# Kernel optimization log

Hardware: AMD Instinct MI355X
Metric: run time of the kernel (lower is better)

Reference implementation:

```python
import jax, jax.numpy as jnp
import numpy as np

RANK = 16
LN_EPS = 1e-5


def _layer_norm(x, eps=LN_EPS):
    mu = jnp.mean(x, axis=-1, keepdims=True)
    var = jnp.var(x, axis=-1, keepdims=True)
    return (x - mu) / jnp.sqrt(var + eps)


def setup_inputs() -> dict:
    key = jax.random.key(0)
    ks = jax.random.split(key, 8)
    B, S, D, M, R = 32, 4096, 160, 16, RANK
    query = jax.random.normal(ks[0], (B, S, D), dtype=jnp.float32)
    interface = jax.random.normal(ks[1], (B, S, D), dtype=jnp.float32)
    memory = jax.random.normal(ks[2], (B, M, D), dtype=jnp.float32)
    sd = 1.0 / np.sqrt(D)
    sr = 1.0 / np.sqrt(R)
    # torch nn.Linear weights: [out_features, in_features]
    W_read_key = jax.random.uniform(ks[3], (R, D), minval=-sd, maxval=sd, dtype=jnp.float32)
    W_read_value = jax.random.uniform(ks[4], (D, R), minval=-sr, maxval=sr, dtype=jnp.float32)
    W_write_key = jax.random.uniform(ks[5], (R, D), minval=-sd, maxval=sd, dtype=jnp.float32)
    W_write_erase = jax.random.uniform(ks[6], (D, R), minval=-sr, maxval=sr, dtype=jnp.float32)
    W_write_add = jax.random.uniform(ks[7], (D, R), minval=-sr, maxval=sr, dtype=jnp.float32)
    return {
        "query": query,
        "interface": interface,
        "memory": memory,
        "W_read_key": W_read_key,
        "W_read_value": W_read_value,
        "W_write_key": W_write_key,
        "W_write_erase": W_write_erase,
        "W_write_add": W_write_add,
    }


def reference(query, interface, memory, W_read_key, W_read_value,
              W_write_key, W_write_erase, W_write_add):
    R = RANK
    # ---- read ----
    q_proj = jnp.einsum('bsd,rd->bsr', query, W_read_key)          # [B,S,R]
    mem_proj = memory[..., :R]                                      # [B,M,R]
    scores = jnp.einsum('bsr,bmr->bsm', q_proj, mem_proj) / jnp.sqrt(jnp.float32(R))
    attn = jax.nn.softmax(scores, axis=-1)                          # [B,S,M]
    content = jnp.einsum('bsm,bmd->bsd', attn, memory)              # [B,S,D]
    read_out = jnp.einsum('bsr,dr->bsd', content[..., :R], W_read_value)
    # ---- write ----
    i_mean = jnp.mean(interface, axis=1)                            # [B,D]
    i_proj = jnp.einsum('bd,rd->br', i_mean, W_write_key)           # [B,R]
    erase = jax.nn.sigmoid(jnp.einsum('br,dr->bd', i_proj, W_write_erase))[:, None, :]
    add = jnp.einsum('br,dr->bd', i_proj, W_write_add)[:, None, :]
    new_memory = _layer_norm(memory * (1.0 - erase) + add)          # [B,M,D]
    return read_out, new_memory
```

## Files before the change

kernel.cpp:

```cpp
#include <hip/hip_runtime.h>
#include <hip/hip_bf16.h>
#include <math.h>

#define NB 32
#define NS 4096
#define ND 160
#define ND4 40
#define NM 16
#define NR 16
#define TPB 128
#define NCB (NS / TPB)

typedef float  f32x4  __attribute__((ext_vector_type(4)));
typedef short  bf16x8 __attribute__((ext_vector_type(8)));
typedef unsigned int u32x4 __attribute__((ext_vector_type(4)));

__device__ __forceinline__ unsigned bfpair(float lo, float hi) {
    union { float f; unsigned u; } a, c;
    a.f = lo; c.f = hi;
    unsigned ua = (a.u + 0x7FFFu + ((a.u >> 16) & 1u)) >> 16;
    unsigned uc = (c.u + 0x7FFFu + ((c.u >> 16) & 1u)) >> 16;
    return (uc << 16) | (ua & 0xFFFFu);
}

__device__ __forceinline__ bf16x8 mkfrag(unsigned w0, unsigned w1,
                                         unsigned w2, unsigned w3) {
    union { u32x4 u; bf16x8 h; } x;
    x.u = (u32x4){w0, w1, w2, w3};
    return x.h;
}

__global__ __launch_bounds__(256) void ulm_read_kernel(
    const float* __restrict__ query,
    const float* __restrict__ iface,
    const float* __restrict__ memory,
    const float* __restrict__ Wrk,
    const float* __restrict__ Wrv,
    float* __restrict__ read_out,
    float* __restrict__ ipart)
{
    __shared__ __align__(16) float sKV[2 * NM * ND];
    __shared__ float sM16[NM * NR];
    __shared__ unsigned sP[4][16 * 10];
    __shared__ float4 sIred[4 * ND4];

    const int t = threadIdx.x;
    const int chunk = blockIdx.x;
    const int b = blockIdx.y;
    const int s0 = chunk * TPB;
    const int w  = t >> 6;
    const int l  = t & 63;
    const int lr = l & 15;
    const int lg = l >> 4;

    sM16[t] = memory[((size_t)b * NM + (t >> 4)) * ND + (t & 15)];
    __syncthreads();

    if (t < ND) {
        float wk[NR], wv[NR];
#pragma unroll
        for (int r = 0; r < NR; ++r) wk[r] = Wrk[r * ND + t];
        const float4* wrv4 = reinterpret_cast<const float4*>(Wrv + t * NR);
#pragma unroll
        for (int j = 0; j < 4; ++j) {
            float4 v = wrv4[j];
            wv[j * 4 + 0] = v.x; wv[j * 4 + 1] = v.y;
            wv[j * 4 + 2] = v.z; wv[j * 4 + 3] = v.w;
        }
#pragma unroll
        for (int m = 0; m < NM; ++m) {
            float aK = 0.f, aV = 0.f;
#pragma unroll
            for (int r = 0; r < NR; ++r) {
                float mv = sM16[m * NR + r];
                aK += mv * wk[r];
                aV += mv * wv[r];
            }
            sKV[m * ND + t]           = aK * 0.25f;
            sKV[NM * ND + m * ND + t] = aV;
        }
    }
    __syncthreads();

    bf16x8 kf[5];
#pragma unroll
    for (int kb = 0; kb < 5; ++kb) {
        const float* src = &sKV[lr * ND + lg * 8 + kb * 32];
        float4 a = *reinterpret_cast<const float4*>(src);
        float4 c = *reinterpret_cast<const float4*>(src + 4);
        kf[kb] = mkfrag(bfpair(a.x, a.y), bfpair(a.z, a.w),
                        bfpair(c.x, c.y), bfpair(c.z, c.w));
    }

    bf16x8 vf[10];
#pragma unroll
    for (int d = 0; d < 10; ++d) {
        if (lg < 2) {
            float f0 = sKV[NM*ND + (lg*8 + 0) * ND + d*16 + lr];
            float f1 = sKV[NM*ND + (lg*8 + 1) * ND + d*16 + lr];
            float f2 = sKV[NM*ND + (lg*8 + 2) * ND + d*16 + lr];
            float f3 = sKV[NM*ND + (lg*8 + 3) * ND + d*16 + lr];
            float f4 = sKV[NM*ND + (lg*8 + 4) * ND + d*16 + lr];
            float f5 = sKV[NM*ND + (lg*8 + 5) * ND + d*16 + lr];
            float f6 = sKV[NM*ND + (lg*8 + 6) * ND + d*16 + lr];
            float f7 = sKV[NM*ND + (lg*8 + 7) * ND + d*16 + lr];
            vf[d] = mkfrag(bfpair(f0, f1), bfpair(f2, f3),
                           bfpair(f4, f5), bfpair(f6, f7));
        } else {
            vf[d] = mkfrag(0u, 0u, 0u, 0u);
        }
    }

    const size_t base = (size_t)b * NS * ND;
    const float4* q4  = reinterpret_cast<const float4*>(query + base) + (size_t)s0 * ND4;
    float4* out4      = reinterpret_cast<float4*>(read_out + base) + (size_t)s0 * ND4;
    const int wtok0 = w * 32;
    unsigned* pl = &sP[w][0];

#pragma unroll 1
    for (int set = 0; set < 2; ++set) {
        const int tok = wtok0 + set * 16 + lr;

        float4 qr[10];
#pragma unroll
        for (int kb = 0; kb < 5; ++kb) {
            qr[2*kb]   = q4[(size_t)tok * ND4 + lg * 2 + kb * 8];
            qr[2*kb+1] = q4[(size_t)tok * ND4 + lg * 2 + kb * 8 + 1];
        }

        f32x4 D = {0.f, 0.f, 0.f, 0.f};
#pragma unroll
        for (int kb = 0; kb < 5; ++kb) {
            bf16x8 qf = mkfrag(bfpair(qr[2*kb].x,   qr[2*kb].y),
                               bfpair(qr[2*kb].z,   qr[2*kb].w),
                               bfpair(qr[2*kb+1].x, qr[2*kb+1].y),
                               bfpair(qr[2*kb+1].z, qr[2*kb+1].w));
            D = __builtin_amdgcn_mfma_f32_16x16x32_bf16(kf[kb], qf, D, 0, 0, 0);
        }

        float mx = fmaxf(fmaxf(D[0], D[1]), fmaxf(D[2], D[3]));
        mx = fmaxf(mx, __shfl_xor(mx, 16));
        mx = fmaxf(mx, __shfl_xor(mx, 32));
        float e0 = __expf(D[0] - mx), e1 = __expf(D[1] - mx);
        float e2 = __expf(D[2] - mx), e3 = __expf(D[3] - mx);
        float sm = e0 + e1 + e2 + e3;
        sm += __shfl_xor(sm, 16);
        sm += __shfl_xor(sm, 32);
        float inv = 1.f / sm;
        e0 *= inv; e1 *= inv; e2 *= inv; e3 *= inv;

        pl[lr * 10 + lg * 2 + 0] = bfpair(e0, e1);
        pl[lr * 10 + lg * 2 + 1] = bfpair(e2, e3);
        asm volatile("s_waitcnt lgkmcnt(0)" ::: "memory");
        int pb = (lg < 2) ? (lr * 10 + lg * 4) : 0;
        bf16x8 pf = mkfrag(pl[pb], pl[pb + 1], pl[pb + 2], pl[pb + 3]);

#pragma unroll
        for (int d = 0; d < 10; ++d) {
            f32x4 D2 = {0.f, 0.f, 0.f, 0.f};
            D2 = __builtin_amdgcn_mfma_f32_16x16x32_bf16(vf[d], pf, D2, 0, 0, 0);
            out4[(size_t)tok * ND4 + d * 4 + lg] =
                make_float4(D2[0], D2[1], D2[2], D2[3]);
        }
    }

    const float4* i4 = reinterpret_cast<const float4*>(iface + base) + (size_t)s0 * ND4;
    const int l8 = l & 7, g8 = l >> 3;
    float4 ia[5];
#pragma unroll
    for (int k = 0; k < 5; ++k) ia[k] = make_float4(0.f, 0.f, 0.f, 0.f);
#pragma unroll
    for (int i = 0; i < 4; ++i) {
        int tk = wtok0 + g8 * 4 + i;
#pragma unroll
        for (int k = 0; k < 5; ++k) {
            float4 v = i4[(size_t)tk * ND4 + l8 + 8 * k];
            ia[k].x += v.x; ia[k].y += v.y; ia[k].z += v.z; ia[k].w += v.w;
        }
    }
#pragma unroll
    for (int k = 0; k < 5; ++k) {
        float x = ia[k].x, y = ia[k].y, z = ia[k].z, u = ia[k].w;
#pragma unroll
        for (int off = 8; off <= 32; off <<= 1) {
            x += __shfl_xor(x, off); y += __shfl_xor(y, off);
            z += __shfl_xor(z, off); u += __shfl_xor(u, off);
        }
        if (l < 8) sIred[w * ND4 + k * 8 + l8] = make_float4(x, y, z, u);
    }
    __syncthreads();
    if (t < ND4) {
        float4 a0 = sIred[t], a1 = sIred[ND4 + t];
        float4 a2 = sIred[2 * ND4 + t], a3 = sIred[3 * ND4 + t];
        float4 tot = make_float4(a0.x + a1.x + a2.x + a3.x,
                                 a0.y + a1.y + a2.y + a3.y,
                                 a0.z + a1.z + a2.z + a3.z,
                                 a0.w + a1.w + a2.w + a3.w);
        reinterpret_cast<float4*>(ipart + ((size_t)(b * NCB + chunk)) * ND)[t] = tot;
    }
}

__global__ __launch_bounds__(256) void ulm_write_kernel(
    const float* __restrict__ memory,
    const float* __restrict__ Wwk,
    const float* __restrict__ Wwe,
    const float* __restrict__ Wwa,
    const float* __restrict__ ipart,
    float* __restrict__ new_mem)
{
    __shared__ float sIm[ND];
    __shared__ float sIp[NR];
    __shared__ float sOmE[ND];
    __shared__ float sAdd[ND];

    const int b = blockIdx.x;
    const int t = threadIdx.x;

    if (t < ND) {
        float acc = 0.f;
#pragma unroll 8
        for (int c = 0; c < NCB; ++c)
            acc += ipart[((size_t)(b * NCB + c)) * ND + t];
        sIm[t] = acc * (1.0f / NS);
    }
    __syncthreads();

    if (t < NR) {
        float acc = 0.f;
        for (int d = 0; d < ND; ++d) acc += sIm[d] * Wwk[t * ND + d];
        sIp[t] = acc;
    }
    __syncthreads();

    if (t < ND) {
        float e = 0.f, a = 0.f;
#pragma unroll
        for (int r = 0; r < NR; ++r) {
            float ip = sIp[r];
            e += ip * Wwe[t * NR + r];
            a += ip * Wwa[t * NR + r];
        }
        sOmE[t] = 1.0f - 1.0f / (1.0f + __expf(-e));
        sAdd[t] = a;
    }
    __syncthreads();

    const int wave = t >> 6, lane = t & 63;
    for (int m = wave; m < NM; m += 4) {
        const float* mrow = memory + ((size_t)b * NM + m) * ND;
        float v0 = mrow[lane] * sOmE[lane] + sAdd[lane];
        float v1 = mrow[lane + 64] * sOmE[lane + 64] + sAdd[lane + 64];
        float v2 = 0.f;
        const bool has2 = lane < 32;
        if (has2) v2 = mrow[lane + 128] * sOmE[lane + 128] + sAdd[lane + 128];
        float s  = v0 + v1 + v2;
        float sq = v0 * v0 + v1 * v1 + v2 * v2;
#pragma unroll
        for (int off = 32; off; off >>= 1) {
            s  += __shfl_xor(s, off);
            sq += __shfl_xor(sq, off);
        }
        float mu   = s * (1.0f / ND);
        float var  = sq * (1.0f / ND) - mu * mu;
        float rstd = rsqrtf(var + 1e-5f);
        float* orow = new_mem + ((size_t)b * NM + m) * ND;
        orow[lane]      = (v0 - mu) * rstd;
        orow[lane + 64] = (v1 - mu) * rstd;
        if (has2) orow[lane + 128] = (v2 - mu) * rstd;
    }
}

extern "C" void kernel_launch(void* const* d_in, const int* in_sizes, int n_in,
                              void* d_out, int out_size, void* d_ws, size_t ws_size,
                              hipStream_t stream) {
    const float* query  = (const float*)d_in[0];
    const float* iface  = (const float*)d_in[1];
    const float* memory = (const float*)d_in[2];
    const float* Wrk    = (const float*)d_in[3];
    const float* Wrv    = (const float*)d_in[4];
    const float* Wwk    = (const float*)d_in[5];
    const float* Wwe    = (const float*)d_in[6];
    const float* Wwa    = (const float*)d_in[7];

    float* read_out = (float*)d_out;
    float* new_mem  = (float*)d_out + (size_t)NB * NS * ND;
    float* ipart    = (float*)d_ws;

    dim3 grid1(NCB, NB);
    ulm_read_kernel<<<grid1, 256, 0, stream>>>(query, iface, memory, Wrk, Wrv,
                                               read_out, ipart);
    ulm_write_kernel<<<NB, 256, 0, stream>>>(memory, Wwk, Wwe, Wwa, ipart, new_mem);
}
```

Before: 56.66 us.

## Hoist K/V fragment folding into a prologue kernel and halve tokens per block

Per-batch folding of memory with the read weights into bf16 MFMA fragments moves into a separate small kernel that writes them to workspace. The main read kernel now loads the prebuilt fragments directly instead of recomputing and converting them in every block. Each block handles 64 tokens with one 16-token set per wave, and the interface loads are issued before the output MFMAs. This removes redundant per-block prologue work and syncs and doubles the block count, at the cost of an extra launch, more workspace and more partial sums for the write kernel to reduce.

```diff
diff --git a/kernel.cpp b/kernel.cpp
--- a/kernel.cpp
+++ b/kernel.cpp
@@ -8,7 +8,7 @@
 #define ND4 40
 #define NM 16
 #define NR 16
-#define TPB 128
+#define TPB 64
 #define NCB (NS / TPB)
 
 typedef float  f32x4  __attribute__((ext_vector_type(4)));
@@ -23,6 +23,10 @@
     return (uc << 16) | (ua & 0xFFFFu);
 }
 
+__device__ __forceinline__ bf16x8 asfrag(u32x4 u) {
+    union { u32x4 u; bf16x8 h; } x; x.u = u; return x.h;
+}
+
 __device__ __forceinline__ bf16x8 mkfrag(unsigned w0, unsigned w1,
                                          unsigned w2, unsigned w3) {
     union { u32x4 u; bf16x8 h; } x;
@@ -30,17 +34,70 @@
     return x.h;
 }
 
+__global__ __launch_bounds__(256) void ulm_fold_kv(
+    const float* __restrict__ memory,
+    const float* __restrict__ Wrk,
+    const float* __restrict__ Wrv,
+    u32x4* __restrict__ kvfrag)
+{
+    __shared__ __align__(16) float sKV[2 * NM * ND];
+    __shared__ float sM16[NM * NR];
+    const int b = blockIdx.x;
+    const int t = threadIdx.x;
+
+    sM16[t] = memory[((size_t)b * NM + (t >> 4)) * ND + (t & 15)];
+    __syncthreads();
+
+    if (t < ND) {
+        float wk[NR], wv[NR];
+#pragma unroll
+        for (int r = 0; r < NR; ++r) wk[r] = Wrk[r * ND + t];
+        const float4* wrv4 = reinterpret_cast<const float4*>(Wrv + t * NR);
+#pragma unroll
+        for (int j = 0; j < 4; ++j) {
+            float4 v = wrv4[j];
+            wv[j * 4 + 0] = v.x; wv[j * 4 + 1] = v.y;
+            wv[j * 4 + 2] = v.z; wv[j * 4 + 3] = v.w;
+        }
+#pragma unroll
+        for (int m = 0; m < NM; ++m) {
+            float aK = 0.f, aV = 0.f;
+#pragma unroll
+            for (int r = 0; r < NR; ++r) {
+                float mv = sM16[m * NR + r];
+                aK += mv * wk[r];
+                aV += mv * wv[r];
+            }
+            sKV[m * ND + t]           = aK * 0.25f;
+            sKV[NM * ND + m * ND + t] = aV;
+        }
+    }
+    __syncthreads();
+
+    u32x4* kb4 = kvfrag + (size_t)b * 640;
+    for (int i = t; i < 320; i += 256) {
+        int kb = i >> 6, l = i & 63, lr = l & 15, lg = l >> 4;
+        const float* s = &sKV[lr * ND + kb * 32 + lg * 8];
+        kb4[i] = (u32x4){bfpair(s[0], s[1]), bfpair(s[2], s[3]),
+                         bfpair(s[4], s[5]), bfpair(s[6], s[7])};
+    }
+    for (int i = t; i < 320; i += 256) {
+        int d = i >> 5, l = i & 31, lr = l & 15, lg = l >> 4;
+        const float* s = &sKV[NM * ND + (lg * 8) * ND + d * 16 + lr];
+        kb4[320 + i] = (u32x4){bfpair(s[0 * ND], s[1 * ND]),
+                               bfpair(s[2 * ND], s[3 * ND]),
+                               bfpair(s[4 * ND], s[5 * ND]),
+                               bfpair(s[6 * ND], s[7 * ND])};
+    }
+}
+
 __global__ __launch_bounds__(256) void ulm_read_kernel(
     const float* __restrict__ query,
     const float* __restrict__ iface,
-    const float* __restrict__ memory,
-    const float* __restrict__ Wrk,
-    const float* __restrict__ Wrv,
+    const u32x4* __restrict__ kvfrag,
     float* __restrict__ read_out,
     float* __restrict__ ipart)
 {
-    __shared__ __align__(16) float sKV[2 * NM * ND];
-    __shared__ float sM16[NM * NR];
     __shared__ unsigned sP[4][16 * 10];
     __shared__ float4 sIred[4 * ND4];
 
@@ -53,134 +110,77 @@
     const int lr = l & 15;
     const int lg = l >> 4;
 
-    sM16[t] = memory[((size_t)b * NM + (t >> 4)) * ND + (t & 15)];
-    __syncthreads();
-
-    if (t < ND) {
-        float wk[NR], wv[NR];
-#pragma unroll
-        for (int r = 0; r < NR; ++r) wk[r] = Wrk[r * ND + t];
-        const float4* wrv4 = reinterpret_cast<const float4*>(Wrv + t * NR);
-#pragma unroll
-        for (int j = 0; j < 4; ++j) {
-            float4 v = wrv4[j];
-            wv[j * 4 + 0] = v.x; wv[j * 4 + 1] = v.y;
-            wv[j * 4 + 2] = v.z; wv[j * 4 + 3] = v.w;
-        }
-#pragma unroll
-        for (int m = 0; m < NM; ++m) {
-            float aK = 0.f, aV = 0.f;
-#pragma unroll
-            for (int r = 0; r < NR; ++r) {
-                float mv = sM16[m * NR + r];
-                aK += mv * wk[r];
-                aV += mv * wv[r];
-            }
-            sKV[m * ND + t]           = aK * 0.25f;
-            sKV[NM * ND + m * ND + t] = aV;
-        }
-    }
-    __syncthreads();
-
-    bf16x8 kf[5];
+    const size_t base = (size_t)b * NS * ND;
+    const int tok = s0 + w * 16 + lr;
+
+    const float4* q4 = reinterpret_cast<const float4*>(query + base);
+    float4 qr[10];
 #pragma unroll
     for (int kb = 0; kb < 5; ++kb) {
-        const float* src = &sKV[lr * ND + lg * 8 + kb * 32];
-        float4 a = *reinterpret_cast<const float4*>(src);
-        float4 c = *reinterpret_cast<const float4*>(src + 4);
-        kf[kb] = mkfrag(bfpair(a.x, a.y), bfpair(a.z, a.w),
-                        bfpair(c.x, c.y), bfpair(c.z, c.w));
-    }
-
-    bf16x8 vf[10];
+        qr[2*kb]   = q4[(size_t)tok * ND4 + lg * 2 + kb * 8];
+        qr[2*kb+1] = q4[(size_t)tok * ND4 + lg * 2 + kb * 8 + 1];
+    }
+
+    const u32x4* kvb = kvfrag + (size_t)b * 640;
+    u32x4 kfu[5];
+#pragma unroll
+    for (int kb = 0; kb < 5; ++kb) kfu[kb] = kvb[kb * 64 + l];
+    u32x4 vfu[10];
+#pragma unroll
+    for (int d = 0; d < 10; ++d)
+        vfu[d] = (lg < 2) ? kvb[320 + d * 32 + (l & 31)]
+                          : (u32x4){0u, 0u, 0u, 0u};
+
+    f32x4 D = {0.f, 0.f, 0.f, 0.f};
+#pragma unroll
+    for (int kb = 0; kb < 5; ++kb) {
+        bf16x8 qf = mkfrag(bfpair(qr[2*kb].x,   qr[2*kb].y),
+                           bfpair(qr[2*kb].z,   qr[2*kb].w),
+                           bfpair(qr[2*kb+1].x, qr[2*kb+1].y),
+                           bfpair(qr[2*kb+1].z, qr[2*kb+1].w));
+        D = __builtin_amdgcn_mfma_f32_16x16x32_bf16(asfrag(kfu[kb]), qf, D, 0, 0, 0);
+    }
+
+    float mx = fmaxf(fmaxf(D[0], D[1]), fmaxf(D[2], D[3]));
+    mx = fmaxf(mx, __shfl_xor(mx, 16));
+    mx = fmaxf(mx, __shfl_xor(mx, 32));
+    float e0 = __expf(D[0] - mx), e1 = __expf(D[1] - mx);
+    float e2 = __expf(D[2] - mx), e3 = __expf(D[3] - mx);
+    float sm = e0 + e1 + e2 + e3;
+    sm += __shfl_xor(sm, 16);
+    sm += __shfl_xor(sm, 32);
+    float inv = 1.f / sm;
+    e0 *= inv; e1 *= inv; e2 *= inv; e3 *= inv;
+
+    unsigned* pl = &sP[w][0];
+    pl[lr * 10 + lg * 2 + 0] = bfpair(e0, e1);
+    pl[lr * 10 + lg * 2 + 1] = bfpair(e2, e3);
+    asm volatile("s_waitcnt lgkmcnt(0)" ::: "memory");
+    int pb = (lg < 2) ? (lr * 10 + lg * 4) : 0;
+    bf16x8 pf = mkfrag(pl[pb], pl[pb + 1], pl[pb + 2], pl[pb + 3]);
+
+    const float4* i4 = reinterpret_cast<const float4*>(iface + base);
+    const int l8 = l & 7, g8 = l >> 3;
+    const int itok = s0 + w * 16 + g8 * 2;
+    float4 iv[10];
+#pragma unroll
+    for (int j = 0; j < 2; ++j)
+#pragma unroll
+        for (int k = 0; k < 5; ++k)
+            iv[j * 5 + k] = i4[(size_t)(itok + j) * ND4 + l8 + 8 * k];
+
+    float4* out4 = reinterpret_cast<float4*>(read_out + base);
 #pragma unroll
     for (int d = 0; d < 10; ++d) {
-        if (lg < 2) {
-            float f0 = sKV[NM*ND + (lg*8 + 0) * ND + d*16 + lr];
-            float f1 = sKV[NM*ND + (lg*8 + 1) * ND + d*16 + lr];
-            float f2 = sKV[NM*ND + (lg*8 + 2) * ND + d*16 + lr];
-            float f3 = sKV[NM*ND + (lg*8 + 3) * ND + d*16 + lr];
-            float f4 = sKV[NM*ND + (lg*8 + 4) * ND + d*16 + lr];
-            float f5 = sKV[NM*ND + (lg*8 + 5) * ND + d*16 + lr];
-            float f6 = sKV[NM*ND + (lg*8 + 6) * ND + d*16 + lr];
-            float f7 = sKV[NM*ND + (lg*8 + 7) * ND + d*16 + lr];
-            vf[d] = mkfrag(bfpair(f0, f1), bfpair(f2, f3),
-                           bfpair(f4, f5), bfpair(f6, f7));
-        } else {
-            vf[d] = mkfrag(0u, 0u, 0u, 0u);
-        }
-    }
-
-    const size_t base = (size_t)b * NS * ND;
-    const float4* q4  = reinterpret_cast<const float4*>(query + base) + (size_t)s0 * ND4;
-    float4* out4      = reinterpret_cast<float4*>(read_out + base) + (size_t)s0 * ND4;
-    const int wtok0 = w * 32;
-    unsigned* pl = &sP[w][0];
-
-#pragma unroll 1
-    for (int set = 0; set < 2; ++set) {
-        const int tok = wtok0 + set * 16 + lr;
-
-        float4 qr[10];
-#pragma unroll
-        for (int kb = 0; kb < 5; ++kb) {
-            qr[2*kb]   = q4[(size_t)tok * ND4 + lg * 2 + kb * 8];
-            qr[2*kb+1] = q4[(size_t)tok * ND4 + lg * 2 + kb * 8 + 1];
-        }
-
-        f32x4 D = {0.f, 0.f, 0.f, 0.f};
-#pragma unroll
-        for (int kb = 0; kb < 5; ++kb) {
-            bf16x8 qf = mkfrag(bfpair(qr[2*kb].x,   qr[2*kb].y),
-                               bfpair(qr[2*kb].z,   qr[2*kb].w),
-                               bfpair(qr[2*kb+1].x, qr[2*kb+1].y),
-                               bfpair(qr[2*kb+1].z, qr[2*kb+1].w));
-            D = __builtin_amdgcn_mfma_f32_16x16x32_bf16(kf[kb], qf, D, 0, 0, 0);
-        }
-
-        float mx = fmaxf(fmaxf(D[0], D[1]), fmaxf(D[2], D[3]));
-        mx = fmaxf(mx, __shfl_xor(mx, 16));
-        mx = fmaxf(mx, __shfl_xor(mx, 32));
-        float e0 = __expf(D[0] - mx), e1 = __expf(D[1] - mx);
-        float e2 = __expf(D[2] - mx), e3 = __expf(D[3] - mx);
-        float sm = e0 + e1 + e2 + e3;
-        sm += __shfl_xor(sm, 16);
-        sm += __shfl_xor(sm, 32);
-        float inv = 1.f / sm;
-        e0 *= inv; e1 *= inv; e2 *= inv; e3 *= inv;
-
-        pl[lr * 10 + lg * 2 + 0] = bfpair(e0, e1);
-        pl[lr * 10 + lg * 2 + 1] = bfpair(e2, e3);
-        asm volatile("s_waitcnt lgkmcnt(0)" ::: "memory");
-        int pb = (lg < 2) ? (lr * 10 + lg * 4) : 0;
-        bf16x8 pf = mkfrag(pl[pb], pl[pb + 1], pl[pb + 2], pl[pb + 3]);
-
-#pragma unroll
-        for (int d = 0; d < 10; ++d) {
-            f32x4 D2 = {0.f, 0.f, 0.f, 0.f};
-            D2 = __builtin_amdgcn_mfma_f32_16x16x32_bf16(vf[d], pf, D2, 0, 0, 0);
-            out4[(size_t)tok * ND4 + d * 4 + lg] =
-                make_float4(D2[0], D2[1], D2[2], D2[3]);
-        }
-    }
-
-    const float4* i4 = reinterpret_cast<const float4*>(iface + base) + (size_t)s0 * ND4;
-    const int l8 = l & 7, g8 = l >> 3;
-    float4 ia[5];
-#pragma unroll
-    for (int k = 0; k < 5; ++k) ia[k] = make_float4(0.f, 0.f, 0.f, 0.f);
-#pragma unroll
-    for (int i = 0; i < 4; ++i) {
-        int tk = wtok0 + g8 * 4 + i;
-#pragma unroll
-        for (int k = 0; k < 5; ++k) {
-            float4 v = i4[(size_t)tk * ND4 + l8 + 8 * k];
-            ia[k].x += v.x; ia[k].y += v.y; ia[k].z += v.z; ia[k].w += v.w;
-        }
-    }
+        f32x4 D2 = {0.f, 0.f, 0.f, 0.f};
+        D2 = __builtin_amdgcn_mfma_f32_16x16x32_bf16(asfrag(vfu[d]), pf, D2, 0, 0, 0);
+        out4[(size_t)tok * ND4 + d * 4 + lg] = make_float4(D2[0], D2[1], D2[2], D2[3]);
+    }
+
 #pragma unroll
     for (int k = 0; k < 5; ++k) {
-        float x = ia[k].x, y = ia[k].y, z = ia[k].z, u = ia[k].w;
+        float x = iv[k].x + iv[5 + k].x, y = iv[k].y + iv[5 + k].y;
+        float z = iv[k].z + iv[5 + k].z, u = iv[k].w + iv[5 + k].w;
 #pragma unroll
         for (int off = 8; off <= 32; off <<= 1) {
             x += __shfl_xor(x, off); y += __shfl_xor(y, off);
@@ -285,9 +285,11 @@
     float* read_out = (float*)d_out;
     float* new_mem  = (float*)d_out + (size_t)NB * NS * ND;
     float* ipart    = (float*)d_ws;
-
+    u32x4* kvfrag   = (u32x4*)((float*)d_ws + (size_t)NB * NCB * ND);
+
+    ulm_fold_kv<<<NB, 256, 0, stream>>>(memory, Wrk, Wrv, kvfrag);
     dim3 grid1(NCB, NB);
-    ulm_read_kernel<<<grid1, 256, 0, stream>>>(query, iface, memory, Wrk, Wrv,
+    ulm_read_kernel<<<grid1, 256, 0, stream>>>(query, iface, kvfrag,
                                                read_out, ipart);
     ulm_write_kernel<<<NB, 256, 0, stream>>>(memory, Wwk, Wwe, Wwa, ipart, new_mem);
 }
```

New measurement: 59.06 us. +4.2%, slower.
